# Kernel tuning notes

Hardware: AMD Instinct MI355X
Metric: run time of the kernel (lower is better)

Reference implementation:

```python
import jax, jax.numpy as jnp
import numpy as np

B, I, O = 1024, 512, 512
EPS = 1e-07
LOG_CLIP = 20.0

def setup_inputs() -> dict:
    key = jax.random.key(0)
    k1, k2, k3, k4 = jax.random.split(key, 4)
    x = jax.random.normal(k1, (B, I), dtype=jnp.float32)
    # match tf.random_normal_initializer(mean, stddev) used in the layer
    w_hat = 0.88 + 0.2 * jax.random.normal(k2, (I, O), dtype=jnp.float32)
    m_hat = 0.5 + 0.2 * jax.random.normal(k3, (I, O), dtype=jnp.float32)
    g = 0.2 * jax.random.normal(k4, (O,), dtype=jnp.float32)
    return {"x": x, "w_hat": w_hat, "m_hat": m_hat, "g": g}

def reference(x, w_hat, m_hat, g):
    w1 = jnp.tanh(w_hat) * jax.nn.sigmoid(m_hat)          # [I, O]
    a = x @ w1                                             # [B, O] additive path
    # multiplicative path: exp(log|x| @ w1), clipped at 20 before exp
    logx = jnp.log(jnp.maximum(jnp.abs(x), EPS))           # [B, I]
    m1 = jnp.exp(jnp.minimum(logx @ w1, LOG_CLIP))         # [B, O]
    # sign-product tracking. TF flattens w1 row-major to [I*O], tiles x
    # O times along axis 1 -> xs[b, k] = x[b, k % I]; so after reshape to
    # [B, O, I], the paired weight magnitude is ws[j, i] = |w1.flat[j*I + i]|.
    ws_oi = jnp.abs(w1.reshape(-1)).reshape(O, I)          # [O, I] (faithful to TF reshape)
    sgn_x = jnp.sign(x)                                    # [B, I]
    sgn = sgn_x[:, None, :] * ws_oi[None, :, :] + (1.0 - ws_oi)[None, :, :]  # [B, O, I]
    ms = jnp.prod(sgn, axis=2)                             # [B, O]
    g1 = jax.nn.sigmoid(g)                                 # [O]
    return g1 * a + (1.0 - g1) * m1 * jnp.clip(ms, -1.0, 1.0)
```

## Files before the change

### kernel.cpp

```cpp
#include <hip/hip_runtime.h>


#define O_N 512
#define I_N 512

typedef _Float16 f16;
typedef _Float16 f16x8 __attribute__((ext_vector_type(8)));
typedef float f32x4 __attribute__((ext_vector_type(4)));

__global__ __launch_bounds__(256) void prep_kernel(const float* __restrict__ x,
                                                   const float* __restrict__ wh,
                                                   const float* __restrict__ mh,
                                                   const float* __restrict__ g,
                                                   f16x8* __restrict__ apx,
                                                   f16x8* __restrict__ apl,
                                                   f16x8* __restrict__ bp,
                                                   float* __restrict__ w1f,
                                                   float* __restrict__ g1v) {
    const int blk = blockIdx.x;
    if (blk < 128) {
        const int t = blk * 256 + threadIdx.x;
        const int lane = t & 63;
        const int tk = (t >> 6) & 15;
        const int tn = t >> 10;
        const int n = tn * 16 + (lane & 15);
        const int k0 = tk * 32 + ((lane >> 4) & 3) * 8;
        f16x8 bf;
#pragma unroll
        for (int j = 0; j < 8; ++j) {
            const int k = k0 + j;
            const float w = tanhf(wh[k * O_N + n]) *
                            (1.0f / (1.0f + expf(-mh[k * O_N + n])));
            w1f[k * O_N + n] = w;
            bf[j] = (f16)w;
        }
        bp[t] = bf;
    } else if (blk < 384) {
        const int t = (blk - 128) * 256 + threadIdx.x;
        const int lane = t & 63;
        const int tk = (t >> 6) & 15;
        const int tm = t >> 10;
        const int m = tm * 16 + (lane & 15);
        const int k0 = tk * 32 + ((lane >> 4) & 3) * 8;
        const float4* x4 = (const float4*)(x + m * I_N + k0);
        const float4 q0 = x4[0], q1 = x4[1];
        const float vx[8] = {q0.x, q0.y, q0.z, q0.w, q1.x, q1.y, q1.z, q1.w};
        f16x8 fx, fl;
#pragma unroll
        for (int j = 0; j < 8; ++j) {
            fx[j] = (f16)vx[j];
            fl[j] = (f16)logf(fmaxf(fabsf(vx[j]), 1e-7f));
        }
        apx[t] = fx;
        apl[t] = fl;
    } else {
        const int o = threadIdx.x;
        g1v[o]       = 1.0f / (1.0f + expf(-g[o]));
        g1v[o + 256] = 1.0f / (1.0f + expf(-g[o + 256]));
    }
}

__global__ __launch_bounds__(256) void nalu_mfma_kernel(const f16x8* __restrict__ apx,
                                                        const f16x8* __restrict__ apl,
                                                        const f16x8* __restrict__ bp,
                                                        const float* __restrict__ g1v,
                                                        const float* __restrict__ w1f,
                                                        const float* __restrict__ x,
                                                        float* __restrict__ out) {
    const int lane = threadIdx.x & 63;
    const int w = threadIdx.x >> 6;
    const int b0 = blockIdx.y * 32 + (w & 1) * 16;
    const int o0 = blockIdx.x * 64 + (w >> 1) * 32;
    const int tm = b0 >> 4;
    const int tn0 = o0 >> 4;

    f32x4 ca0 = {0.f, 0.f, 0.f, 0.f}, ca1 = ca0, cs0 = ca0, cs1 = ca0;

    const f16x8* pax = apx + tm * (16 * 64) + lane;
    const f16x8* pal = apl + tm * (16 * 64) + lane;
    const f16x8* pb0 = bp + tn0 * (16 * 64) + lane;
    const f16x8* pb1 = bp + (tn0 + 1) * (16 * 64) + lane;

#pragma unroll 4
    for (int tk = 0; tk < 16; ++tk) {
        const f16x8 ax = pax[tk * 64];
        const f16x8 al = pal[tk * 64];
        const f16x8 bf0 = pb0[tk * 64];
        const f16x8 bf1 = pb1[tk * 64];
        ca0 = __builtin_amdgcn_mfma_f32_16x16x32_f16(ax, bf0, ca0, 0, 0, 0);
        ca1 = __builtin_amdgcn_mfma_f32_16x16x32_f16(ax, bf1, ca1, 0, 0, 0);
        cs0 = __builtin_amdgcn_mfma_f32_16x16x32_f16(al, bf0, cs0, 0, 0, 0);
        cs1 = __builtin_amdgcn_mfma_f32_16x16x32_f16(al, bf1, cs1, 0, 0, 0);
    }

    const int col = lane & 15;
    const int rq = (lane >> 4) * 4;
#pragma unroll
    for (int t = 0; t < 2; ++t) {
        const int o = o0 + t * 16 + col;
        const float g1 = g1v[o];
        const float omg = 1.0f - g1;
        const f32x4 ca = t ? ca1 : ca0;
        const f32x4 cs = t ? cs1 : cs0;
#pragma unroll
        for (int r = 0; r < 4; ++r) {
            const int b = b0 + rq + r;
            const float sv = cs[r];
            const float m1 = expf(fminf(sv, 20.0f));
            float msv = 1.0f;
            if (sv > -80.0f) {
                float p = 1.0f;
                for (int i = 0; i < I_N; ++i) {
                    const float wv = fabsf(w1f[o * I_N + i]);
                    const float xv = x[b * I_N + i];
                    const float sg = (xv > 0.f) ? 1.f : ((xv < 0.f) ? -1.f : 0.f);
                    p *= sg * wv + (1.0f - wv);
                }
                msv = fminf(fmaxf(p, -1.0f), 1.0f);
            }
            out[b * O_N + o] = g1 * ca[r] + omg * m1 * msv;
        }
    }
}

extern "C" void kernel_launch(void* const* d_in, const int* in_sizes, int n_in,
                              void* d_out, int out_size, void* d_ws, size_t ws_size,
                              hipStream_t stream) {
    const float* x  = (const float*)d_in[0];
    const float* wh = (const float*)d_in[1];
    const float* mh = (const float*)d_in[2];
    const float* g  = (const float*)d_in[3];
    float* out = (float*)d_out;

    char* ws = (char*)d_ws;
    f16x8* apx = (f16x8*)ws;
    f16x8* apl = (f16x8*)(ws + (1u << 20));
    f16x8* bp  = (f16x8*)(ws + (2u << 20));
    float* w1f = (float*)(ws + (5u << 19));
    float* g1v = (float*)(ws + (7u << 19));

    prep_kernel<<<385, 256, 0, stream>>>(x, wh, mh, g, apx, apl, bp, w1f, g1v);
    nalu_mfma_kernel<<<dim3(8, 32), 256, 0, stream>>>(apx, apl, bp, g1v, w1f, x, out);
}
```

Measured before the change: 73.89 us.

## Coalesce weight prep via LDS transpose, drop fp32 w1 buffer, halve MFMA tiles

```diff
diff --git a/kernel.cpp b/kernel.cpp
--- a/kernel.cpp
+++ b/kernel.cpp
@@ -3,123 +3,130 @@
 
 #define O_N 512
 #define I_N 512
+#define B_N 1024
 
 typedef _Float16 f16;
 typedef _Float16 f16x8 __attribute__((ext_vector_type(8)));
 typedef float f32x4 __attribute__((ext_vector_type(4)));
 
+__device__ __forceinline__ float fast_sigmoid(float v) {
+    return 1.0f / (1.0f + __expf(-v));
+}
+__device__ __forceinline__ float fast_tanh(float v) {
+    return 1.0f - 2.0f / (1.0f + __expf(2.0f * v));
+}
+
 __global__ __launch_bounds__(256) void prep_kernel(const float* __restrict__ x,
                                                    const float* __restrict__ wh,
                                                    const float* __restrict__ mh,
-                                                   const float* __restrict__ g,
                                                    f16x8* __restrict__ apx,
                                                    f16x8* __restrict__ apl,
-                                                   f16x8* __restrict__ bp,
-                                                   float* __restrict__ w1f,
-                                                   float* __restrict__ g1v) {
-    const int blk = blockIdx.x;
-    if (blk < 128) {
-        const int t = blk * 256 + threadIdx.x;
-        const int lane = t & 63;
-        const int tk = (t >> 6) & 15;
-        const int tn = t >> 10;
-        const int n = tn * 16 + (lane & 15);
-        const int k0 = tk * 32 + ((lane >> 4) & 3) * 8;
+                                                   f16x8* __restrict__ bp) {
+    const int tid = threadIdx.x;
+    if (blockIdx.x < 128) {
+        __shared__ f16 lt[32][72];
+        const int kb = blockIdx.x >> 3;
+        const int nb = blockIdx.x & 7;
+        const int r  = tid >> 3;
+        const int c0 = (tid & 7) * 8;
+        const int base = (kb * 32 + r) * O_N + nb * 64 + c0;
+        const float4* w4 = (const float4*)(wh + base);
+        const float4* m4 = (const float4*)(mh + base);
+        const float4 wa = w4[0], wb = w4[1], ma = m4[0], mb = m4[1];
+        f16x8 row;
+        row[0] = (f16)(fast_tanh(wa.x) * fast_sigmoid(ma.x));
+        row[1] = (f16)(fast_tanh(wa.y) * fast_sigmoid(ma.y));
+        row[2] = (f16)(fast_tanh(wa.z) * fast_sigmoid(ma.z));
+        row[3] = (f16)(fast_tanh(wa.w) * fast_sigmoid(ma.w));
+        row[4] = (f16)(fast_tanh(wb.x) * fast_sigmoid(mb.x));
+        row[5] = (f16)(fast_tanh(wb.y) * fast_sigmoid(mb.y));
+        row[6] = (f16)(fast_tanh(wb.z) * fast_sigmoid(mb.z));
+        row[7] = (f16)(fast_tanh(wb.w) * fast_sigmoid(mb.w));
+        *(f16x8*)&lt[r][c0] = row;
+        __syncthreads();
+        const int fl  = tid & 63;
+        const int tnl = tid >> 6;
+        const int nl  = tnl * 16 + (fl & 15);
+        const int k0  = (fl >> 4) * 8;
         f16x8 bf;
 #pragma unroll
-        for (int j = 0; j < 8; ++j) {
-            const int k = k0 + j;
-            const float w = tanhf(wh[k * O_N + n]) *
-                            (1.0f / (1.0f + expf(-mh[k * O_N + n])));
-            w1f[k * O_N + n] = w;
-            bf[j] = (f16)w;
-        }
-        bp[t] = bf;
-    } else if (blk < 384) {
-        const int t = (blk - 128) * 256 + threadIdx.x;
-        const int lane = t & 63;
+        for (int j = 0; j < 8; ++j) bf[j] = lt[k0 + j][nl];
+        const int tn_g = nb * 4 + tnl;
+        bp[tn_g * 1024 + kb * 64 + fl] = bf;
+    } else {
+        const int t  = (blockIdx.x - 128) * 256 + tid;
+        const int fl = t & 63;
         const int tk = (t >> 6) & 15;
         const int tm = t >> 10;
-        const int m = tm * 16 + (lane & 15);
-        const int k0 = tk * 32 + ((lane >> 4) & 3) * 8;
+        const int m  = tm * 16 + (fl & 15);
+        const int k0 = tk * 32 + (fl >> 4) * 8;
         const float4* x4 = (const float4*)(x + m * I_N + k0);
         const float4 q0 = x4[0], q1 = x4[1];
         const float vx[8] = {q0.x, q0.y, q0.z, q0.w, q1.x, q1.y, q1.z, q1.w};
-        f16x8 fx, fl;
+        f16x8 fx, fv;
 #pragma unroll
         for (int j = 0; j < 8; ++j) {
             fx[j] = (f16)vx[j];
-            fl[j] = (f16)logf(fmaxf(fabsf(vx[j]), 1e-7f));
+            fv[j] = (f16)__logf(fmaxf(fabsf(vx[j]), 1e-7f));
         }
         apx[t] = fx;
-        apl[t] = fl;
-    } else {
-        const int o = threadIdx.x;
-        g1v[o]       = 1.0f / (1.0f + expf(-g[o]));
-        g1v[o + 256] = 1.0f / (1.0f + expf(-g[o + 256]));
+        apl[t] = fv;
     }
 }
 
 __global__ __launch_bounds__(256) void nalu_mfma_kernel(const f16x8* __restrict__ apx,
                                                         const f16x8* __restrict__ apl,
                                                         const f16x8* __restrict__ bp,
-                                                        const float* __restrict__ g1v,
-                                                        const float* __restrict__ w1f,
+                                                        const float* __restrict__ g,
                                                         const float* __restrict__ x,
+                                                        const float* __restrict__ wh,
+                                                        const float* __restrict__ mh,
                                                         float* __restrict__ out) {
     const int lane = threadIdx.x & 63;
-    const int w = threadIdx.x >> 6;
-    const int b0 = blockIdx.y * 32 + (w & 1) * 16;
-    const int o0 = blockIdx.x * 64 + (w >> 1) * 32;
-    const int tm = b0 >> 4;
-    const int tn0 = o0 >> 4;
+    const int w    = threadIdx.x >> 6;
+    const int b0   = blockIdx.y * 32 + (w & 1) * 16;
+    const int o0   = blockIdx.x * 32 + (w >> 1) * 16;
+    const int tm   = b0 >> 4;
+    const int tn   = o0 >> 4;
 
-    f32x4 ca0 = {0.f, 0.f, 0.f, 0.f}, ca1 = ca0, cs0 = ca0, cs1 = ca0;
+    f32x4 ca = {0.f, 0.f, 0.f, 0.f}, cs = ca;
 
-    const f16x8* pax = apx + tm * (16 * 64) + lane;
-    const f16x8* pal = apl + tm * (16 * 64) + lane;
-    const f16x8* pb0 = bp + tn0 * (16 * 64) + lane;
-    const f16x8* pb1 = bp + (tn0 + 1) * (16 * 64) + lane;
+    const f16x8* pax = apx + tm * 1024 + lane;
+    const f16x8* pal = apl + tm * 1024 + lane;
+    const f16x8* pbp = bp  + tn * 1024 + lane;
 
-#pragma unroll 4
+#pragma unroll 8
     for (int tk = 0; tk < 16; ++tk) {
         const f16x8 ax = pax[tk * 64];
         const f16x8 al = pal[tk * 64];
-        const f16x8 bf0 = pb0[tk * 64];
-        const f16x8 bf1 = pb1[tk * 64];
-        ca0 = __builtin_amdgcn_mfma_f32_16x16x32_f16(ax, bf0, ca0, 0, 0, 0);
-        ca1 = __builtin_amdgcn_mfma_f32_16x16x32_f16(ax, bf1, ca1, 0, 0, 0);
-        cs0 = __builtin_amdgcn_mfma_f32_16x16x32_f16(al, bf0, cs0, 0, 0, 0);
-        cs1 = __builtin_amdgcn_mfma_f32_16x16x32_f16(al, bf1, cs1, 0, 0, 0);
+        const f16x8 bf = pbp[tk * 64];
+        ca = __builtin_amdgcn_mfma_f32_16x16x32_f16(ax, bf, ca, 0, 0, 0);
+        cs = __builtin_amdgcn_mfma_f32_16x16x32_f16(al, bf, cs, 0, 0, 0);
     }
 
     const int col = lane & 15;
-    const int rq = (lane >> 4) * 4;
+    const int rq  = (lane >> 4) * 4;
+    const int o   = o0 + col;
+    const float g1  = fast_sigmoid(g[o]);
+    const float omg = 1.0f - g1;
 #pragma unroll
-    for (int t = 0; t < 2; ++t) {
-        const int o = o0 + t * 16 + col;
-        const float g1 = g1v[o];
-        const float omg = 1.0f - g1;
-        const f32x4 ca = t ? ca1 : ca0;
-        const f32x4 cs = t ? cs1 : cs0;
-#pragma unroll
-        for (int r = 0; r < 4; ++r) {
-            const int b = b0 + rq + r;
-            const float sv = cs[r];
-            const float m1 = expf(fminf(sv, 20.0f));
-            float msv = 1.0f;
-            if (sv > -80.0f) {
-                float p = 1.0f;
-                for (int i = 0; i < I_N; ++i) {
-                    const float wv = fabsf(w1f[o * I_N + i]);
-                    const float xv = x[b * I_N + i];
-                    const float sg = (xv > 0.f) ? 1.f : ((xv < 0.f) ? -1.f : 0.f);
-                    p *= sg * wv + (1.0f - wv);
-                }
-                msv = fminf(fmaxf(p, -1.0f), 1.0f);
+    for (int r = 0; r < 4; ++r) {
+        const int b = b0 + rq + r;
+        const float sv = cs[r];
+        const float m1 = __expf(fminf(sv, 20.0f));
+        float msv = 1.0f;
+        if (sv > -80.0f) {
+            float p = 1.0f;
+            for (int i = 0; i < I_N; ++i) {
+                const float wv = fabsf(fast_tanh(wh[o * I_N + i]) *
+                                       fast_sigmoid(mh[o * I_N + i]));
+                const float xv = x[b * I_N + i];
+                const float sg = (xv > 0.f) ? 1.f : ((xv < 0.f) ? -1.f : 0.f);
+                p *= sg * wv + (1.0f - wv);
             }
-            out[b * O_N + o] = g1 * ca[r] + omg * m1 * msv;
+            msv = fminf(fmaxf(p, -1.0f), 1.0f);
         }
+        out[b * O_N + o] = g1 * ca[r] + omg * m1 * msv;
     }
 }
 
@@ -136,9 +143,7 @@
     f16x8* apx = (f16x8*)ws;
     f16x8* apl = (f16x8*)(ws + (1u << 20));
     f16x8* bp  = (f16x8*)(ws + (2u << 20));
-    float* w1f = (float*)(ws + (5u << 19));
-    float* g1v = (float*)(ws + (7u << 19));
 
-    prep_kernel<<<385, 256, 0, stream>>>(x, wh, mh, g, apx, apl, bp, w1f, g1v);
-    nalu_mfma_kernel<<<dim3(8, 32), 256, 0, stream>>>(apx, apl, bp, g1v, w1f, x, out);
+    prep_kernel<<<384, 256, 0, stream>>>(x, wh, mh, apx, apl, bp);
+    nalu_mfma_kernel<<<dim3(16, 32), 256, 0, stream>>>(apx, apl, bp, g, x, wh, mh, out);
 }
```

Measured after the change: 68.82 us. 1.07x faster.
